# Kernel tuning notes

Hardware: AMD Instinct MI355X
Metric: run time of the kernel (lower is better)

The kernel has to match this reference:

```python
import jax, jax.numpy as jnp
import numpy as np

K = 5           # kernel_size
STRIDE = 1
DILATION = 1
PAD = 2         # padding='same': total = dilation*(K-1) = 4, left = 2, right = 2 (reflect mode)


def setup_inputs() -> dict:
    key = jax.random.key(0)
    k1, k2, k3, k4 = jax.random.split(key, 4)
    B, C_in, C_out, L = 8, 64, 64, 16384
    x = jax.random.normal(k1, (B, C_in, L), dtype=jnp.float32)
    # offsets broadcast over channels: (B, 1, L_out, K); L_out == L for padding='same'
    offsets = jax.random.normal(k2, (B, 1, L, K), dtype=jnp.float32)
    weight = jax.random.normal(k3, (C_out, C_in, K), dtype=jnp.float32) * (1.0 / np.sqrt(C_in * K))
    bias = jax.random.normal(k4, (C_out,), dtype=jnp.float32) * 0.05
    return {"x": x, "offsets": offsets, "weight": weight, "bias": bias}


def _deform_interp(xp, offsets):
    # xp: (B, C, Lp) padded input; offsets: (B, 1, Lo, K)
    B, C, Lp = xp.shape
    Lo, Kk = offsets.shape[-2], offsets.shape[-1]
    t0 = (STRIDE * jnp.arange(Lo, dtype=xp.dtype))[:, None]          # base sample positions
    dil = (DILATION * jnp.arange(Kk, dtype=xp.dtype))[None, :]       # dilated kernel positions
    T = jnp.clip(t0 + dil + offsets, 0.0, float(Lp - 1))             # (B, 1, Lo, K)
    i0 = jnp.clip(jnp.floor(T).astype(jnp.int32), 0, Lp - 2)
    frac = T - i0.astype(xp.dtype)                                   # linear-interp weight
    i0b = jnp.broadcast_to(i0, (B, C, Lo, Kk)).reshape(B, C, Lo * Kk)
    g0 = jnp.take_along_axis(xp, i0b, axis=-1).reshape(B, C, Lo, Kk)
    g1 = jnp.take_along_axis(xp, i0b + 1, axis=-1).reshape(B, C, Lo, Kk)
    return g0 * (1.0 - frac) + g1 * frac                             # (B, C, Lo, K)


def reference(x, offsets, weight, bias):
    # 'same' padding with reflect mode
    xp = jnp.pad(x, ((0, 0), (0, 0), (PAD, PAD)), mode="reflect")
    v = _deform_interp(xp, offsets)                                  # (B, C, Lo, K)
    # flatten(-2,-1) + conv1d(stride=K, groups=1) == contraction over (c, k) per output pos
    out = jnp.einsum("bclk,ock->bol", v, weight) + bias[None, :, None]
    return out
```

## Files before the change

kernel.cpp:

```cpp
#include <hip/hip_runtime.h>

#define BATCH 8
#define CIN   64
#define COUT  64
#define LEN   16384
#define KS    5
#define PADW  2
#define LP    (LEN + 2*PADW)
#define TTB   128
#define XROWS 104
#define XM    14

typedef __attribute__((ext_vector_type(8)))  short short8;
typedef __attribute__((ext_vector_type(4)))  float f32x4;
typedef __attribute__((ext_vector_type(8)))  unsigned short ushort8;

__device__ __forceinline__ unsigned short bf16r(float f) {
    unsigned u = __builtin_bit_cast(unsigned, f);
    u += 0x7FFF + ((u >> 16) & 1);
    return (unsigned short)(u >> 16);
}
__device__ __forceinline__ unsigned fpack(float a, float b) {
    unsigned ua = __builtin_bit_cast(unsigned, a) + 0x8000u;
    unsigned ub = __builtin_bit_cast(unsigned, b) + 0x8000u;
    return __builtin_amdgcn_perm(ub, ua, 0x07060302);
}
__device__ __forceinline__ int reflmap(int s) {
    return (s < PADW) ? (PADW - s) : ((s < LEN + PADW) ? (s - PADW) : (2*LEN - s));
}

__global__ void wfrag_kernel(const float* __restrict__ w, unsigned short* __restrict__ wf) {
    int el = blockIdx.x * 256 + threadIdx.x;
    int e    = el & 7;
    int lane = (el >> 3) & 63;
    int kk   = (el >> 9) % 10;
    int ot   = el / 5120;
    int o    = ot * 16 + (lane & 15);
    int kg   = kk * 32 + ((lane >> 4) << 3) + e;
    int ktap = kg >> 6;
    int c    = kg & 63;
    wf[el] = bf16r(w[(o * 64 + c) * 5 + ktap]);
}

__global__ __launch_bounds__(256, 4) void deform_mfma_kernel(
    const float* __restrict__ x, const float* __restrict__ offs,
    const unsigned short* __restrict__ wf, const float* __restrict__ bias,
    float* __restrict__ out)
{
    __shared__ __align__(16) unsigned short xtl[2][XROWS * 64];

    const int tid = threadIdx.x;
    const int bid = blockIdx.x;
    const int bt  = (bid & 7) * 128 + (bid >> 3);
    const int b   = bt >> 7;
    const int T0  = (bt & 127) * TTB;
    const int w   = tid >> 6;
    const int lane = tid & 63;
    const int pl  = lane & 15;
    const int s   = lane >> 4;

    const float* xb0 = x + (size_t)b * CIN * LEN;
    const unsigned short* wfl = wf + (size_t)lane * 8;

    float of[2][KS];
    #pragma unroll
    for (int it = 0; it < 2; ++it) {
        const int tc = T0 + it * 64 + w * 16 + pl;
        #pragma unroll
        for (int k = 0; k < KS; ++k)
            of[it][k] = offs[((size_t)(b * LEN + tc)) * KS + k];
    }

    float4 vA0[2], vA1[2], vB0[2], vB1[2];
    int stg_fast;

#define STAGE_LOAD(t0s)                                                        \
    stg_fast = ((t0s) >= 16 && (t0s) + 88 <= LEN);                             \
    if (stg_fast) {                                                            \
        const float* src0 = xb0 + ((t0s) - 16);                                \
        _Pragma("unroll")                                                      \
        for (int rep = 0; rep < 2; ++rep) {                                    \
            int task = rep * 256 + tid;                                        \
            if (task < 416) {                                                  \
                int c2 = task / 13, q = task - c2 * 13;                        \
                const float* p0 = src0 + (size_t)(2 * c2) * LEN + 8 * q;       \
                vA0[rep] = *(const float4*)p0;                                 \
                vA1[rep] = *(const float4*)(p0 + 4);                           \
                vB0[rep] = *(const float4*)(p0 + LEN);                         \
                vB1[rep] = *(const float4*)(p0 + LEN + 4);                     \
            }                                                                  \
        }                                                                      \
    }

#define STAGE_WRITE(dst, t0s)                                                  \
    if (stg_fast) {                                                            \
        _Pragma("unroll")                                                      \
        for (int rep = 0; rep < 2; ++rep) {                                    \
            int task = rep * 256 + tid;                                        \
            if (task < 416) {                                                  \
                int c2 = task / 13, q = task - c2 * 13;                        \
                float av[8] = {vA0[rep].x, vA0[rep].y, vA0[rep].z, vA0[rep].w, \
                               vA1[rep].x, vA1[rep].y, vA1[rep].z, vA1[rep].w};\
                float bv[8] = {vB0[rep].x, vB0[rep].y, vB0[rep].z, vB0[rep].w, \
                               vB1[rep].x, vB1[rep].y, vB1[rep].z, vB1[rep].w};\
                _Pragma("unroll")                                              \
                for (int i = 0; i < 8; ++i) {                                  \
                    int r = 8 * q + i;                                         \
                    *(unsigned*)((char*)(dst) + r * 128 +                      \
                        ((4 * c2) ^ ((r & 7) << 4))) = fpack(av[i], bv[i]);    \
                }                                                              \
            }                                                                  \
        }                                                                      \
    } else {                                                                   \
        const int S0e = (t0s) - XM;                                            \
        _Pragma("unroll")                                                      \
        for (int rep = 0; rep < 26; ++rep) {                                   \
            int idx = rep * 256 + tid;                    \
            int r = idx >> 6, c = idx & 63;                                    \
            int sp = min(max(S0e + r, 0), LP - 1);                             \
            *(unsigned short*)((char*)(dst) + r * 128 +                        \
                ((2 * c) ^ ((r & 7) << 4))) = bf16r(xb0[(size_t)c * LEN + reflmap(sp)]); \
        }                                                                      \
    }

#define LERPW(dst, w0, w1, f)                                                  \
    {                                                                          \
        float g0a = __builtin_bit_cast(float, (w0) << 16);                     \
        float g1a = __builtin_bit_cast(float, (w1) << 16);                     \
        float g0b = __builtin_bit_cast(float, (w0) & 0xFFFF0000u);             \
        float g1b = __builtin_bit_cast(float, (w1) & 0xFFFF0000u);             \
        dst = fpack(fmaf(f, g1a - g0a, g0a), fmaf(f, g1b - g0b, g0b));         \
    }

#define GST(kk, CHECKED)                                                       \
    {                                                                          \
        const int k = (kk) >> 1;                                               \
        const int m = (((kk) & 1) << 2) + s;                   \
        const float f = frr[k];                                                \
        uint4 pw;                                                              \
        if (!(CHECKED) || (unsigned)r0r[k] <= (unsigned)(XROWS - 2)) {         \
            const int r0 = r0r[k], r1 = r0r[k] + 1;                            \
            uint4 u0 = *(const uint4*)((const char*)xbuf + r0 * 128 + ((m * 16) ^ ((r0 & 7) << 4))); \
            uint4 u1 = *(const uint4*)((const char*)xbuf + r1 * 128 + ((m * 16) ^ ((r1 & 7) << 4))); \
            LERPW(pw.x, u0.x, u1.x, f) LERPW(pw.y, u0.y, u1.y, f)              \
            LERPW(pw.z, u0.z, u1.z, f) LERPW(pw.w, u0.w, u1.w, f)              \
        } else {                                                               \
            int j0 = reflmap(i0r[k]), j1 = reflmap(i0r[k] + 1);                \
            const float* xc = xb0 + (size_t)(m << 3) * LEN;                    \
            unsigned pv[4];                                                    \
            _Pragma("unroll")                                                  \
            for (int e = 0; e < 4; ++e) {                                      \
                float ga0 = xc[j0], ga1 = xc[j1];                              \
                float lo = fmaf(f, ga1 - ga0, ga0);                            \
                float gb0 = xc[LEN + j0], gb1 = xc[LEN + j1];                  \
                float hi = fmaf(f, gb1 - gb0, gb0);                            \
                pv[e] = fpack(lo, hi);                                         \
                xc += 2 * LEN;                                                 \
            }                                                                  \
            pw = uint4{pv[0], pv[1], pv[2], pv[3]};                            \
        }                                                                      \
        short8 bv = __builtin_bit_cast(short8, pw);                            \
        short8 a0 = *(const short8*)&wfl[(0 * 10 + (kk)) * 512];               \
        short8 a1 = *(const short8*)&wfl[(1 * 10 + (kk)) * 512];               \
        short8 a2 = *(const short8*)&wfl[(2 * 10 + (kk)) * 512];               \
        short8 a3 = *(const short8*)&wfl[(3 * 10 + (kk)) * 512];               \
        acc0 = __builtin_amdgcn_mfma_f32_16x16x32_bf16(a0, bv, acc0, 0, 0, 0); \
        acc1 = __builtin_amdgcn_mfma_f32_16x16x32_bf16(a1, bv, acc1, 0, 0, 0); \
        acc2 = __builtin_amdgcn_mfma_f32_16x16x32_bf16(a2, bv, acc2, 0, 0, 0); \
        acc3 = __builtin_amdgcn_mfma_f32_16x16x32_bf16(a3, bv, acc3, 0, 0, 0); \
    }

#define SUBTILE(it)                                                            \
    {                                                                          \
        const int t0s = T0 + (it) * 64;                                        \
        if ((it) == 0) { STAGE_LOAD(t0s + 64); }    \
        const int S0 = t0s - XM;                                               \
        const int tc = t0s + w * 16 + pl;                                      \
        int i0r[KS]; float frr[KS]; int r0r[KS]; bool fastg = true;            \
        _Pragma("unroll")                                                      \
        for (int k = 0; k < KS; ++k) {                                         \
            float T = (float)(tc + k) + of[it][k];                             \
            T = fminf(fmaxf(T, 0.0f), (float)(LP - 1));                        \
            int i0 = (int)floorf(T);                                           \
            i0 = min(i0, LP - 2); i0 = max(i0, 0);                             \
            i0r[k] = i0; frr[k] = T - (float)i0; r0r[k] = i0 - S0;             \
            fastg = fastg && ((unsigned)(i0 - S0) <= (unsigned)(XROWS - 2));   \
        }                                                                      \
        const unsigned short* xbuf = xtl[(it)];                                \
        f32x4 acc0 = {}, acc1 = {}, acc2 = {}, acc3 = {};                      \
        if (fastg) { GST(0,0) GST(1,0) GST(2,0) GST(3,0) GST(4,0)              \
                     GST(5,0) GST(6,0) GST(7,0) GST(8,0) GST(9,0) }            \
        else       { GST(0,1) GST(1,1) GST(2,1) GST(3,1) GST(4,1)              \
                     GST(5,1) GST(6,1) GST(7,1) GST(8,1) GST(9,1) }            \
        _Pragma("unroll")                                                      \
        for (int ot = 0; ot < 4; ++ot) {                                       \
            const f32x4 a = (ot==0)?acc0:(ot==1)?acc1:(ot==2)?acc2:acc3;       \
            _Pragma("unroll")                                                  \
            for (int r = 0; r < 4; ++r) {                                      \
                int o = ot * 16 + s * 4 + r;                                   \
                out[((size_t)(b * COUT + o)) * LEN + tc] = a[r] + bias[o];     \
            }                                                                  \
        }                                                                      \
        if ((it) == 0) { STAGE_WRITE(xtl[1], t0s + 64); __syncthreads(); }     \
    }

    STAGE_LOAD(T0);
    STAGE_WRITE(xtl[0], T0);
    __syncthreads();

    SUBTILE(0)
    SUBTILE(1)

#undef SUBTILE
#undef GST
#undef LERPW
#undef STAGE_WRITE
#undef STAGE_LOAD
}

extern "C" void kernel_launch(void* const* d_in, const int* in_sizes, int n_in,
                              void* d_out, int out_size, void* d_ws, size_t ws_size,
                              hipStream_t stream) {
    const float* x    = (const float*)d_in[0];
    const float* offs = (const float*)d_in[1];
    const float* w    = (const float*)d_in[2];
    const float* bias = (const float*)d_in[3];
    float* out = (float*)d_out;
    unsigned short* wf = (unsigned short*)d_ws;

    wfrag_kernel<<<80, 256, 0, stream>>>(w, wf);
    deform_mfma_kernel<<<BATCH * (LEN / TTB), 256, 0, stream>>>(x, offs, wf, bias, out);
}
```

Baseline: 34.54 us.

## Fuse both subtiles into one pass sharing weight fragments across two MFMA streams

Stages both 64-position input tiles into shared memory up front behind a single barrier, then computes both subtiles together. Each weight fragment is loaded once and fed to two MFMAs, one per subtile, with separate accumulator sets. This halves weight-fragment loads and removes the serialized second stage and barrier. The cost is doubled accumulators and gather registers, which may raise register pressure and reduce occupancy.

```diff
diff --git a/kernel.cpp b/kernel.cpp
--- a/kernel.cpp
+++ b/kernel.cpp
@@ -13,7 +13,6 @@
 
 typedef __attribute__((ext_vector_type(8)))  short short8;
 typedef __attribute__((ext_vector_type(4)))  float f32x4;
-typedef __attribute__((ext_vector_type(8)))  unsigned short ushort8;
 
 __device__ __forceinline__ unsigned short bf16r(float f) {
     unsigned u = __builtin_bit_cast(unsigned, f);
@@ -62,13 +61,13 @@
     const float* xb0 = x + (size_t)b * CIN * LEN;
     const unsigned short* wfl = wf + (size_t)lane * 8;
 
-    float of[2][KS];
-    #pragma unroll
-    for (int it = 0; it < 2; ++it) {
-        const int tc = T0 + it * 64 + w * 16 + pl;
-        #pragma unroll
-        for (int k = 0; k < KS; ++k)
-            of[it][k] = offs[((size_t)(b * LEN + tc)) * KS + k];
+    float of0[KS], of1[KS];
+    {
+        const int tcா = T0 + w * 16 + pl;
+        #pragma unroll
+        for (int k = 0; k < KS; ++k) of0[k] = offs[((size_t)(b * LEN + tcா)) * KS + k];
+        #pragma unroll
+        for (int k = 0; k < KS; ++k) of1[k] = offs[((size_t)(b * LEN + tcா + 64)) * KS + k];
     }
 
     float4 vA0[2], vA1[2], vB0[2], vB1[2];
@@ -80,7 +79,7 @@
         const float* src0 = xb0 + ((t0s) - 16);                                \
         _Pragma("unroll")                                                      \
         for (int rep = 0; rep < 2; ++rep) {                                    \
-            int task = rep * 256 + tid;                                        \
+            int task = rep * 256 + tid;            \
             if (task < 416) {                                                  \
                 int c2 = task / 13, q = task - c2 * 13;                        \
                 const float* p0 = src0 + (size_t)(2 * c2) * LEN + 8 * q;       \
@@ -132,87 +131,145 @@
         dst = fpack(fmaf(f, g1a - g0a, g0a), fmaf(f, g1b - g0b, g0b));         \
     }
 
-#define GST(kk, CHECKED)                                                       \
-    {                                                                          \
-        const int k = (kk) >> 1;                                               \
-        const int m = (((kk) & 1) << 2) + s;                   \
-        const float f = frr[k];                                                \
-        uint4 pw;                                                              \
-        if (!(CHECKED) || (unsigned)r0r[k] <= (unsigned)(XROWS - 2)) {         \
-            const int r0 = r0r[k], r1 = r0r[k] + 1;                            \
-            uint4 u0 = *(const uint4*)((const char*)xbuf + r0 * 128 + ((m * 16) ^ ((r0 & 7) << 4))); \
-            uint4 u1 = *(const uint4*)((const char*)xbuf + r1 * 128 + ((m * 16) ^ ((r1 & 7) << 4))); \
-            LERPW(pw.x, u0.x, u1.x, f) LERPW(pw.y, u0.y, u1.y, f)              \
-            LERPW(pw.z, u0.z, u1.z, f) LERPW(pw.w, u0.w, u1.w, f)              \
-        } else {                                                               \
-            int j0 = reflmap(i0r[k]), j1 = reflmap(i0r[k] + 1);                \
-            const float* xc = xb0 + (size_t)(m << 3) * LEN;                    \
-            unsigned pv[4];                                                    \
-            _Pragma("unroll")                                                  \
-            for (int e = 0; e < 4; ++e) {                                      \
-                float ga0 = xc[j0], ga1 = xc[j1];                              \
-                float lo = fmaf(f, ga1 - ga0, ga0);                            \
-                float gb0 = xc[LEN + j0], gb1 = xc[LEN + j1];                  \
-                float hi = fmaf(f, gb1 - gb0, gb0);                            \
-                pv[e] = fpack(lo, hi);                                         \
-                xc += 2 * LEN;                                                 \
-            }                                                                  \
-            pw = uint4{pv[0], pv[1], pv[2], pv[3]};                            \
-        }                                                                      \
-        short8 bv = __builtin_bit_cast(short8, pw);                            \
+#define GATHF(pw, XB, R0A, FRA, k, mm)                                         \
+    {                                                                          \
+        const int r0 = R0A[k], r1 = r0 + 1;                                    \
+        const float f = FRA[k];                                                \
+        uint4 u0 = *(const uint4*)((const char*)(XB) + r0 * 128 + ((mm) ^ ((r0 & 7) << 4))); \
+        uint4 u1 = *(const uint4*)((const char*)(XB) + r1 * 128 + ((mm) ^ ((r1 & 7) << 4))); \
+        LERPW(pw.x, u0.x, u1.x, f) LERPW(pw.y, u0.y, u1.y, f)                  \
+        LERPW(pw.z, u0.z, u1.z, f) LERPW(pw.w, u0.w, u1.w, f)                  \
+    }
+
+#define GATHS(pw, I0A, FRA, k, m)                                              \
+    {                                                                          \
+        const float f = FRA[k];                                                \
+        int j0 = reflmap(I0A[k]), j1 = reflmap(I0A[k] + 1);                    \
+        const float* xc = xb0 + (size_t)((m) << 3) * LEN;                      \
+        unsigned pv[4];                                                        \
+        _Pragma("unroll")                                                      \
+        for (int e = 0; e < 4; ++e) {                                          \
+            float ga0 = xc[j0], ga1 = xc[j1];                                  \
+            float lo = fmaf(f, ga1 - ga0, ga0);                                \
+            float gb0 = xc[LEN + j0], gb1 = xc[LEN + j1];                      \
+            float hi = fmaf(f, gb1 - gb0, gb0);                                \
+            pv[e] = fpack(lo, hi);                                             \
+            xc += 2 * LEN;                                                     \
+        }                                                                      \
+        pw = uint4{pv[0], pv[1], pv[2], pv[3]};                                \
+    }
+
+#define MFMA8(kk, pw0, pw1)                                                    \
+    {                                                                          \
+        short8 bv0 = __builtin_bit_cast(short8, pw0);                          \
+        short8 bv1 = __builtin_bit_cast(short8, pw1);                          \
         short8 a0 = *(const short8*)&wfl[(0 * 10 + (kk)) * 512];               \
         short8 a1 = *(const short8*)&wfl[(1 * 10 + (kk)) * 512];               \
         short8 a2 = *(const short8*)&wfl[(2 * 10 + (kk)) * 512];               \
         short8 a3 = *(const short8*)&wfl[(3 * 10 + (kk)) * 512];               \
-        acc0 = __builtin_amdgcn_mfma_f32_16x16x32_bf16(a0, bv, acc0, 0, 0, 0); \
-        acc1 = __builtin_amdgcn_mfma_f32_16x16x32_bf16(a1, bv, acc1, 0, 0, 0); \
-        acc2 = __builtin_amdgcn_mfma_f32_16x16x32_bf16(a2, bv, acc2, 0, 0, 0); \
-        acc3 = __builtin_amdgcn_mfma_f32_16x16x32_bf16(a3, bv, acc3, 0, 0, 0); \
-    }
-
-#define SUBTILE(it)                                                            \
-    {                                                                          \
-        const int t0s = T0 + (it) * 64;                                        \
-        if ((it) == 0) { STAGE_LOAD(t0s + 64); }    \
-        const int S0 = t0s - XM;                                               \
-        const int tc = t0s + w * 16 + pl;                                      \
-        int i0r[KS]; float frr[KS]; int r0r[KS]; bool fastg = true;            \
-        _Pragma("unroll")                                                      \
-        for (int k = 0; k < KS; ++k) {                                         \
-            float T = (float)(tc + k) + of[it][k];                             \
-            T = fminf(fmaxf(T, 0.0f), (float)(LP - 1));                        \
-            int i0 = (int)floorf(T);                                           \
-            i0 = min(i0, LP - 2); i0 = max(i0, 0);                             \
-            i0r[k] = i0; frr[k] = T - (float)i0; r0r[k] = i0 - S0;             \
-            fastg = fastg && ((unsigned)(i0 - S0) <= (unsigned)(XROWS - 2));   \
-        }                                                                      \
-        const unsigned short* xbuf = xtl[(it)];                                \
-        f32x4 acc0 = {}, acc1 = {}, acc2 = {}, acc3 = {};                      \
-        if (fastg) { GST(0,0) GST(1,0) GST(2,0) GST(3,0) GST(4,0)              \
-                     GST(5,0) GST(6,0) GST(7,0) GST(8,0) GST(9,0) }            \
-        else       { GST(0,1) GST(1,1) GST(2,1) GST(3,1) GST(4,1)              \
-                     GST(5,1) GST(6,1) GST(7,1) GST(8,1) GST(9,1) }            \
-        _Pragma("unroll")                                                      \
-        for (int ot = 0; ot < 4; ++ot) {                                       \
-            const f32x4 a = (ot==0)?acc0:(ot==1)?acc1:(ot==2)?acc2:acc3;       \
-            _Pragma("unroll")                                                  \
-            for (int r = 0; r < 4; ++r) {                                      \
-                int o = ot * 16 + s * 4 + r;                                   \
-                out[((size_t)(b * COUT + o)) * LEN + tc] = a[r] + bias[o];     \
-            }                                                                  \
-        }                                                                      \
-        if ((it) == 0) { STAGE_WRITE(xtl[1], t0s + 64); __syncthreads(); }     \
+        accA0 = __builtin_amdgcn_mfma_f32_16x16x32_bf16(a0, bv0, accA0, 0, 0, 0); \
+        accB0 = __builtin_amdgcn_mfma_f32_16x16x32_bf16(a0, bv1, accB0, 0, 0, 0); \
+        accA1 = __builtin_amdgcn_mfma_f32_16x16x32_bf16(a1, bv0, accA1, 0, 0, 0); \
+        accB1 = __builtin_amdgcn_mfma_f32_16x16x32_bf16(a1, bv1, accB1, 0, 0, 0); \
+        accA2 = __builtin_amdgcn_mfma_f32_16x16x32_bf16(a2, bv0, accA2, 0, 0, 0); \
+        accB2 = __builtin_amdgcn_mfma_f32_16x16x32_bf16(a2, bv1, accB2, 0, 0, 0); \
+        accA3 = __builtin_amdgcn_mfma_f32_16x16x32_bf16(a3, bv0, accA3, 0, 0, 0); \
+        accB3 = __builtin_amdgcn_mfma_f32_16x16x32_bf16(a3, bv1, accB3, 0, 0, 0); \
+    }
+
+#define FUSED(kk)                                                              \
+    {                                                                          \
+        const int k  = (kk) >> 1;                                              \
+        const int mm = ((((kk) & 1) << 2) + s) * 16;                           \
+        uint4 pw0, pw1;                                                        \
+        GATHF(pw0, xtl[0], r00, fr0, k, mm)                                    \
+        GATHF(pw1, xtl[1], r01, fr1, k, mm)                                    \
+        MFMA8(kk, pw0, pw1)                                                    \
+    }
+
+#define CHECKED1(kk, pw, R0A, I0A, FRA, XB)                                    \
+    {                                                                          \
+        const int k = (kk) >> 1;                                               \
+        const int m = (((kk) & 1) << 2) + s;                                   \
+        if ((unsigned)R0A[k] <= (unsigned)(XROWS - 2)) {                       \
+            GATHF(pw, XB, R0A, FRA, k, m * 16)                                 \
+        } else {                                                               \
+            GATHS(pw, I0A, FRA, k, m)                                          \
+        }                                                                      \
+    }
+
+#define FUSEDC(kk)                                                             \
+    {                                                                          \
+        uint4 pw0, pw1;                                                        \
+        CHECKED1(kk, pw0, r00, i00, fr0, xtl[0])                               \
+        CHECKED1(kk, pw1, r01, i01, fr1, xtl[1])                               \
+        MFMA8(kk, pw0, pw1)                                                    \
     }
 
     STAGE_LOAD(T0);
     STAGE_WRITE(xtl[0], T0);
+    STAGE_LOAD(T0 + 64);
+
+    int i00[KS], i01[KS], r00[KS], r01[KS];
+    float fr0[KS], fr1[KS];
+    bool fastg = true;
+    {
+        const int tc0 = T0 + w * 16 + pl;
+        #pragma unroll
+        for (int k = 0; k < KS; ++k) {
+            float T = (float)(tc0 + k) + of0[k];
+            T = fminf(fmaxf(T, 0.0f), (float)(LP - 1));
+            int i0 = (int)floorf(T);
+            i0 = min(i0, LP - 2); i0 = max(i0, 0);
+            i00[k] = i0; fr0[k] = T - (float)i0; r00[k] = i0 - (T0 - XM);
+            fastg = fastg && ((unsigned)r00[k] <= (unsigned)(XROWS - 2));
+        }
+        #pragma unroll
+        for (int k = 0; k < KS; ++k) {
+            float T = (float)(tc0 + 64 + k) + of1[k];
+            T = fminf(fmaxf(T, 0.0f), (float)(LP - 1));
+            int i0 = (int)floorf(T);
+            i0 = min(i0, LP - 2); i0 = max(i0, 0);
+            i01[k] = i0; fr1[k] = T - (float)i0; r01[k] = i0 - (T0 + 64 - XM);
+            fastg = fastg && ((unsigned)r01[k] <= (unsigned)(XROWS - 2));
+        }
+    }
+
+    STAGE_WRITE(xtl[1], T0 + 64);
     __syncthreads();
 
-    SUBTILE(0)
-    SUBTILE(1)
-
-#undef SUBTILE
-#undef GST
+    f32x4 accA0 = {}, accA1 = {}, accA2 = {}, accA3 = {};
+    f32x4 accB0 = {}, accB1 = {}, accB2 = {}, accB3 = {};
+    if (fastg) {
+        FUSED(0) FUSED(1) FUSED(2) FUSED(3) FUSED(4)
+        FUSED(5) FUSED(6) FUSED(7) FUSED(8) FUSED(9)
+    } else {
+        FUSEDC(0) FUSEDC(1) FUSEDC(2) FUSEDC(3) FUSEDC(4)
+        FUSEDC(5) FUSEDC(6) FUSEDC(7) FUSEDC(8) FUSEDC(9)
+    }
+
+    {
+        const int tc0 = T0 + w * 16 + pl;
+        #pragma unroll
+        for (int ot = 0; ot < 4; ++ot) {
+            const f32x4 aA = (ot==0)?accA0:(ot==1)?accA1:(ot==2)?accA2:accA3;
+            const f32x4 aB = (ot==0)?accB0:(ot==1)?accB1:(ot==2)?accB2:accB3;
+            #pragma unroll
+            for (int r = 0; r < 4; ++r) {
+                int o = ot * 16 + s * 4 + r;
+                float bvv = bias[o];
+                float* op = out + ((size_t)(b * COUT + o)) * LEN + tc0;
+                op[0]  = aA[r] + bvv;
+                op[64] = aB[r] + bvv;
+            }
+        }
+    }
+#undef FUSEDC
+#undef CHECKED1
+#undef FUSED
+#undef MFMA8
+#undef GATHS
+#undef GATHF
 #undef LERPW
 #undef STAGE_WRITE
 #undef STAGE_LOAD
```

Result: faster. 31.83 us (-7.8%).
